# Kernel optimization log

Measured on AMD Instinct MI355X. Metric: run time of the kernel, lower is better.

The kernel has to match this reference:

```python
import jax, jax.numpy as jnp
import numpy as np


def _sobel(img):
    # replicate-pad then Sobel cross-correlation (matches torch conv2d with wx, wy)
    p = jnp.pad(img, ((0, 0), (0, 0), (1, 1), (1, 1)), mode='edge')
    dx = ((p[:, :, 0:-2, 2:] - p[:, :, 0:-2, 0:-2])
          + 2.0 * (p[:, :, 1:-1, 2:] - p[:, :, 1:-1, 0:-2])
          + (p[:, :, 2:, 2:] - p[:, :, 2:, 0:-2]))
    dy = ((p[:, :, 2:, 0:-2] - p[:, :, 0:-2, 0:-2])
          + 2.0 * (p[:, :, 2:, 1:-1] - p[:, :, 0:-2, 1:-1])
          + (p[:, :, 2:, 2:] - p[:, :, 0:-2, 2:]))
    return dx, dy


def _compute_normal(vertex):
    # normal = normalize(dV/dx x dV/dy); zero out pixels at global min/max depth
    dx, dy = _sobel(vertex)
    n = jnp.cross(dx, dy, axis=1)                      # [B,3,H,W]
    mag = jnp.sqrt(jnp.sum(n * n, axis=1, keepdims=True) + 1e-16)
    n = n / (mag + 1e-8)
    depth = vertex[:, 2:3]
    invalid = (depth == depth.min()) | (depth == depth.max())
    return jnp.where(invalid, 0.0, n)


def _warp(feat, u, v):
    # bilinear sampling of feat [B,C,H,W] at (u,v) [B,N] -> [B,C,N]
    B, C, H, W = feat.shape
    u = jnp.clip(u, 0.0, W - 1.0)
    v = jnp.clip(v, 0.0, H - 1.0)
    u0 = jnp.floor(u); v0 = jnp.floor(v)
    wu = u - u0; wv = v - v0
    u0i = u0.astype(jnp.int32); v0i = v0.astype(jnp.int32)
    u1i = jnp.minimum(u0i + 1, W - 1); v1i = jnp.minimum(v0i + 1, H - 1)
    flat = feat.reshape(B, C, H * W)
    N = u.shape[-1]
    def g(ui, vi):
        idx = (vi * W + ui)[:, None, :]
        return jnp.take_along_axis(flat, jnp.broadcast_to(idx, (B, C, N)), axis=2)
    return (g(u0i, v0i) * ((1 - wu) * (1 - wv))[:, None]
            + g(u1i, v0i) * (wu * (1 - wv))[:, None]
            + g(u0i, v1i) * ((1 - wu) * wv)[:, None]
            + g(u1i, v1i) * (wu * wv)[:, None])


def _skew(v):  # [B,3] -> [B,3,3]
    x, y, z = v[..., 0], v[..., 1], v[..., 2]
    O = jnp.zeros_like(x)
    return jnp.stack([jnp.stack([O, -z, y], -1),
                      jnp.stack([z, O, -x], -1),
                      jnp.stack([-y, x, O], -1)], -2)


def _twist2mat(w):  # Rodrigues: so(3) [B,3] -> SO(3) [B,3,3]
    th = jnp.sqrt(jnp.sum(w * w, -1, keepdims=True) + 1e-24)
    Kv = _skew(w / th)
    th = th[..., None]
    I = jnp.eye(3, dtype=w.dtype)
    return I + jnp.sin(th) * Kv + (1.0 - jnp.cos(th)) * (Kv @ Kv)


def _icp_forward(depth0, depth1, K, R, t, max_iter=3):
    B, _, H, W = depth0.shape
    fx, fy, cx, cy = [K[:, i:i + 1] for i in range(4)]  # each [B,1]
    uu = jnp.arange(W, dtype=depth0.dtype)
    vv = jnp.arange(H, dtype=depth0.dtype)
    px = (uu[None, None, None, :] - cx[:, :, None, None]) / fx[:, :, None, None]
    py = (vv[None, None, :, None] - cy[:, :, None, None]) / fy[:, :, None, None]
    px = jnp.broadcast_to(px, (B, 1, H, W))
    py = jnp.broadcast_to(py, (B, 1, H, W))
    vertex0 = jnp.concatenate([px * depth0, py * depth0, depth0], 1)  # [B,3,H,W]
    vertex1 = jnp.concatenate([px * depth1, py * depth1, depth1], 1)
    normal0 = _compute_normal(vertex0)
    normal1 = _compute_normal(vertex1)
    N = H * W
    V0 = vertex0.reshape(B, 3, N)
    N0 = normal0.reshape(B, 3, N)
    P0 = V0.transpose(0, 2, 1)                          # [B,N,3]
    dpt0 = vertex0[:, 2].reshape(B, N)
    sigma_z = 0.0012 + 0.0019 * (dpt0 - 0.4) ** 2       # depth noise model
    eye6 = jnp.eye(6, dtype=depth0.dtype)
    for _ in range(max_iter):
        v0to1 = R @ V0 + t                               # [B,3,N]
        x_, y_, s_ = v0to1[:, 0], v0to1[:, 1], v0to1[:, 2]
        u_ = x_ / s_ * fx + cx
        v_ = y_ / s_ * fy + cy
        inviews = (u_ > 0) & (u_ < W - 1) & (v_ > 0) & (v_ < H - 1)
        rV1 = _warp(vertex1, u_, v_)                     # [B,3,N]
        rN1 = _warp(normal1, u_, v_)
        diff = v0to1 - rV1
        dnorm = jnp.sqrt(jnp.sum(diff * diff, axis=1) + 1e-16)
        occ = (~inviews) | (dnorm > 0.1)                 # [B,N]
        res = jnp.sum(rN1 * diff, axis=1)                # point-to-plane residual [B,N]
        NtC = jnp.einsum('bcn,bck->bnk', rN1, R)         # n_r^T R, [B,N,3]
        # n^T [p]_x == cross(n^T R, p)
        J = jnp.concatenate([jnp.cross(NtC, P0), -NtC], -1)  # [B,N,6]
        # sigma ~ |n_r . (R e_z)| * sigma_z (depth noise projected on normal)
        ndot = jnp.abs(jnp.sum(rN1 * R[:, :, 2][:, :, None], axis=1))
        sigma = ndot * sigma_z + 1e-3
        w_res = res / (sigma + 1e-8)
        J = -J / (sigma + 1e-8)[..., None]
        w_res = jnp.where(occ, 0.0, w_res)
        J = jnp.where(occ[..., None], 0.0, J)
        JtWJ = jnp.einsum('bnk,bnl->bkl', J, J)          # [B,6,6]
        JtR = jnp.einsum('bnk,bn->bk', J, w_res)[..., None]  # [B,6,1]
        tr = jnp.trace(JtWJ, axis1=1, axis2=2)
        Hlm = JtWJ + (tr * 1e-6)[:, None, None] * eye6   # LM damping
        xi = jnp.linalg.inv(Hlm) @ JtR                   # [B,6,1]
        dR = _twist2mat(-xi[:, :3, 0])
        dt = -(dR @ xi[:, 3:])
        R, t = R @ dR, R @ dt + t                        # inverse-compositional update
    weights = jnp.ones((B, 1, H, W), dtype=depth0.dtype)
    return R, t, weights


def setup_inputs() -> dict:
    key = jax.random.key(0)
    B, H, W = 16, 480, 640
    k1, k2, k3, k4 = jax.random.split(key, 4)
    TWO_PI = 6.2831853
    xs = jnp.linspace(0.0, 1.0, W, dtype=jnp.float32)
    ys = jnp.linspace(0.0, 1.0, H, dtype=jnp.float32)
    phase = jax.random.uniform(k1, (B, 1, 1, 1), minval=0.0, maxval=TWO_PI)
    # smooth positive depth surface so ICP inlier test keeps valid pixels
    depth0 = (2.0 + 0.5 * jnp.sin(TWO_PI * 3.0 * xs[None, None, None, :] + phase)
              * jnp.cos(TWO_PI * 2.0 * ys[None, None, :, None])).astype(jnp.float32)
    depth1 = depth0 + 0.01 * jax.random.normal(k2, (B, 1, H, W), dtype=jnp.float32)
    K = jnp.tile(jnp.array([[525.0, 525.0, 319.5, 239.5]], dtype=jnp.float32), (B, 1))
    w = 0.005 * jax.random.normal(k3, (B, 3), dtype=jnp.float32)
    R = _twist2mat(w)                                    # near-identity initial rotation
    t = 0.005 * jax.random.normal(k4, (B, 3, 1), dtype=jnp.float32)
    return {"depth0": depth0, "depth1": depth1, "K": K, "R": R, "t": t}


def reference(depth0, depth1, K, R, t):
    return _icp_forward(depth0, depth1, K, R, t, max_iter=3)
```

## Files before the change

### kernel.cpp

```cpp
#include <hip/hip_runtime.h>

#define IMH 480
#define IMW 640
#define HW (IMH*IMW)
#define NB 16

#define BPB 100
#define TPX 4
#define GROUPS 3
#define THREADS_PB (BPB*256)
#define GSTRIDE (THREADS_PB*TPX)
#define GROWS (GSTRIDE/IMW)

#define MMB 512

__device__ inline unsigned fenc(float x){
    unsigned u = __float_as_uint(x);
    return (u & 0x80000000u) ? ~u : (u | 0x80000000u);
}
__device__ inline float fdec(unsigned e){
    unsigned u = (e & 0x80000000u) ? (e & 0x7FFFFFFFu) : ~e;
    return __uint_as_float(u);
}

__global__ __launch_bounds__(256) void minmax_kernel(const float4* __restrict__ d,
                                                     unsigned* __restrict__ pmin,
                                                     unsigned* __restrict__ pmax,
                                                     float* __restrict__ acc){
    if (blockIdx.x == 0){
        for (int k = threadIdx.x; k < NB*27; k += 256) acc[k] = 0.f;
    }
    unsigned lmin = 0xFFFFFFFFu, lmax = 0u;
    const int total4 = NB*HW/4;
    for (int i = blockIdx.x*256 + threadIdx.x; i < total4; i += MMB*256){
        float4 v = d[i];
        unsigned e0 = fenc(v.x), e1 = fenc(v.y), e2 = fenc(v.z), e3 = fenc(v.w);
        lmin = min(lmin, min(min(e0,e1), min(e2,e3)));
        lmax = max(lmax, max(max(e0,e1), max(e2,e3)));
    }
    #pragma unroll
    for (int off = 32; off; off >>= 1){
        lmin = min(lmin, (unsigned)__shfl_down((int)lmin, off));
        lmax = max(lmax, (unsigned)__shfl_down((int)lmax, off));
    }
    __shared__ unsigned smin[4], smax[4];
    int wave = threadIdx.x >> 6, lane = threadIdx.x & 63;
    if (lane == 0){ smin[wave] = lmin; smax[wave] = lmax; }
    __syncthreads();
    if (threadIdx.x == 0){
        pmin[blockIdx.x] = min(min(smin[0],smin[1]), min(smin[2],smin[3]));
        pmax[blockIdx.x] = max(max(smax[0],smax[1]), max(smax[2],smax[3]));
    }
}

__global__ __launch_bounds__(256) void normal_kernel(const float* __restrict__ depth1,
                                                     const float* __restrict__ Kp,
                                                     const unsigned* __restrict__ pmin,
                                                     const unsigned* __restrict__ pmax,
                                                     uint4* __restrict__ nrm4,
                                                     float4* __restrict__ weights4){
    __shared__ unsigned sred[8];
    __shared__ unsigned sfin[2];
    {
        unsigned vmin = min(pmin[threadIdx.x], pmin[threadIdx.x + 256]);
        unsigned vmax = max(pmax[threadIdx.x], pmax[threadIdx.x + 256]);
        #pragma unroll
        for (int off = 32; off; off >>= 1){
            vmin = min(vmin, (unsigned)__shfl_down((int)vmin, off));
            vmax = max(vmax, (unsigned)__shfl_down((int)vmax, off));
        }
        int wave = threadIdx.x >> 6, lane = threadIdx.x & 63;
        if (lane == 0){ sred[wave] = vmin; sred[4+wave] = vmax; }
        __syncthreads();
        if (threadIdx.x == 0){
            sfin[0] = min(min(sred[0],sred[1]), min(sred[2],sred[3]));
            sfin[1] = max(max(sred[4],sred[5]), max(sred[6],sred[7]));
        }
        __syncthreads();
    }
    const float dmin = fdec(sfin[0]), dmax = fdec(sfin[1]);

    const int b = blockIdx.y;
    const int t = blockIdx.x*256 + threadIdx.x;
    const int gpr = IMW/4;
    const int r = t / gpr;
    const int c0 = (t - r*gpr)*4;
    const float fx = Kp[b*4+0], fy = Kp[b*4+1], cx = Kp[b*4+2], cy = Kp[b*4+3];
    const float inv_fx = 1.f/fx, inv_fy = 1.f/fy;
    const float* __restrict__ d = depth1 + (size_t)b*HW;
    const int rm = max(r-1,0), rp = min(r+1,IMH-1);

    float wm[6], wc[6], wp[6];
    {
        const float* rowm = d + rm*IMW + c0;
        const float* rowc = d + r *IMW + c0;
        const float* rowp = d + rp*IMW + c0;
        float4 vm = *(const float4*)rowm;
        float4 vc = *(const float4*)rowc;
        float4 vp = *(const float4*)rowp;
        wm[1]=vm.x; wm[2]=vm.y; wm[3]=vm.z; wm[4]=vm.w;
        wc[1]=vc.x; wc[2]=vc.y; wc[3]=vc.z; wc[4]=vc.w;
        wp[1]=vp.x; wp[2]=vp.y; wp[3]=vp.z; wp[4]=vp.w;
        bool hasL = (c0 > 0), hasR = (c0+4 < IMW);
        wm[0] = hasL ? rowm[-1] : vm.x;   wm[5] = hasR ? rowm[4] : vm.w;
        wc[0] = hasL ? rowc[-1] : vc.x;   wc[5] = hasR ? rowc[4] : vc.w;
        wp[0] = hasL ? rowp[-1] : vp.x;   wp[5] = hasR ? rowp[4] : vp.w;
    }
    float pxw[6];
    #pragma unroll
    for (int k=0;k<6;k++){
        int cc = min(max(c0-1+k, 0), IMW-1);
        pxw[k] = ((float)cc - cx)*inv_fx;
    }
    const float pym = ((float)rm - cy)*inv_fy;
    const float pyc = ((float)r  - cy)*inv_fy;
    const float pyp = ((float)rp - cy)*inv_fy;

    unsigned packed[4];
    #pragma unroll
    for (int j=0;j<4;j++){
        float aL = wm[j],  aC = wm[j+1], aR = wm[j+2];
        float bL = wc[j],               bR = wc[j+2];
        float cL = wp[j],  cC = wp[j+1], cR = wp[j+2];
        float pL = pxw[j], pC = pxw[j+1], pR = pxw[j+2];

        float dx0 = (pR*aR - pL*aL) + 2.f*(pR*bR - pL*bL) + (pR*cR - pL*cL);
        float dx1 = pym*(aR - aL) + 2.f*pyc*(bR - bL) + pyp*(cR - cL);
        float dx2 = (aR - aL) + 2.f*(bR - bL) + (cR - cL);
        float dy0 = pL*(cL - aL) + 2.f*pC*(cC - aC) + pR*(cR - aR);
        float dy1 = (pyp*cL - pym*aL) + 2.f*(pyp*cC - pym*aC) + (pyp*cR - pym*aR);
        float dy2 = (cL - aL) + 2.f*(cC - aC) + (cR - aR);

        float nx = dx1*dy2 - dx2*dy1;
        float ny = dx2*dy0 - dx0*dy2;
        float nz = dx0*dy1 - dx1*dy0;
        float mag = sqrtf(nx*nx + ny*ny + nz*nz + 1e-16f);
        float inv = __builtin_amdgcn_rcpf(mag + 1e-8f);
        nx *= inv; ny *= inv; nz *= inv;

        float dc = wc[j+1];
        if (dc == dmin || dc == dmax){ nx = 0.f; ny = 0.f; nz = 0.f; }

        int qx = (int)rintf(nx*127.f) + 127;
        int qy = (int)rintf(ny*127.f) + 127;
        int qz = (int)rintf(nz*127.f) + 127;
        packed[j] = ((unsigned)qx) | ((unsigned)qy << 8) | ((unsigned)qz << 16);
    }

    size_t o4 = (size_t)b*(HW/4) + (size_t)r*gpr + (c0>>2);
    nrm4[o4] = make_uint4(packed[0], packed[1], packed[2], packed[3]);
    weights4[o4] = make_float4(1.f,1.f,1.f,1.f);
}

__global__ __launch_bounds__(256) void iter_kernel(const float4* __restrict__ depth0_v4,
                                                   const float* __restrict__ depth1,
                                                   const unsigned* __restrict__ nrm,
                                                   const float* __restrict__ Kp,
                                                   const float* __restrict__ stateR,
                                                   const float* __restrict__ statet,
                                                   float* __restrict__ acc){
    const int b = blockIdx.y;
    const float fx = Kp[b*4+0], fy = Kp[b*4+1], cx = Kp[b*4+2], cy = Kp[b*4+3];
    const float inv_fx = 1.f/fx, inv_fy = 1.f/fy;
    float Rm[9];
    #pragma unroll
    for (int i=0;i<9;i++) Rm[i] = stateR[b*9+i];
    float tv[3];
    #pragma unroll
    for (int i=0;i<3;i++) tv[i] = statet[b*3+i];

    const float4* __restrict__ d0v = depth0_v4 + (size_t)b*(HW/4);
    const float* __restrict__ d1   = depth1 + (size_t)b*HW;
    const unsigned* __restrict__ nb_ = nrm + (size_t)b*HW;

    float accv[27];
    #pragma unroll
    for (int i=0;i<27;i++) accv[i] = 0.f;

    const int tid = blockIdx.x*256 + threadIdx.x;
    const int base0 = tid*TPX;
    const int c0 = base0 % IMW;
    const int r0 = base0 / IMW;
    const float px_base = ((float)c0 - cx)*inv_fx;
    const float py0 = ((float)r0 - cy)*inv_fy;
    const float py_step = (float)GROWS*inv_fy;
    const float inv127 = 1.f/127.f;

    #pragma unroll
    for (int g = 0; g < GROUPS; g++){
        float4 d4 = d0v[tid + g*THREADS_PB];
        float dd[4] = {d4.x, d4.y, d4.z, d4.w};
        float pyv = py0 + (float)g*py_step;

        #pragma unroll
        for (int j = 0; j < TPX; j++){
            float d0 = dd[j];
            float V0x = (px_base + (float)j*inv_fx)*d0;
            float V0y = pyv*d0;
            float V0z = d0;

            float X = Rm[0]*V0x + Rm[1]*V0y + Rm[2]*V0z + tv[0];
            float Y = Rm[3]*V0x + Rm[4]*V0y + Rm[5]*V0z + tv[1];
            float Z = Rm[6]*V0x + Rm[7]*V0y + Rm[8]*V0z + tv[2];
            float invZ = __builtin_amdgcn_rcpf(Z);
            float uu = X*invZ*fx + cx;
            float vv = Y*invZ*fy + cy;

            bool inview = (uu > 0.f) && (uu < (float)(IMW-1)) && (vv > 0.f) && (vv < (float)(IMH-1));

            float J0=0.f,J1=0.f,J2=0.f,J3=0.f,J4=0.f,J5=0.f,wres=0.f;
            if (inview){
                float u0f = floorf(uu), v0f = floorf(vv);
                int u0 = (int)u0f, v0 = (int)v0f;
                float wu = uu - u0f, wv = vv - v0f;
                float w00 = (1.f-wu)*(1.f-wv), w10 = wu*(1.f-wv), w01 = (1.f-wu)*wv, w11 = wu*wv;
                int i00 = v0*IMW + u0;

                float d00 = d1[i00], d10 = d1[i00+1], d01 = d1[i00+IMW], d11 = d1[i00+IMW+1];
                unsigned h00 = nb_[i00], h10 = nb_[i00+1], h01 = nb_[i00+IMW], h11 = nb_[i00+IMW+1];

                float pxa = (u0f - cx)*inv_fx, pxb = pxa + inv_fx;
                float pya = (v0f - cy)*inv_fy, pyb = pya + inv_fy;
                float a = w00*d00, bb = w10*d10, cc = w01*d01, ee = w11*d11;
                float rVz = (a + bb) + (cc + ee);
                float rVx = (a + cc)*pxa + (bb + ee)*pxb;
                float rVy = (a + bb)*pya + (cc + ee)*pyb;

                float q00x = (float)(h00 & 0xFFu);
                float q00y = (float)((h00 >> 8) & 0xFFu);
                float q00z = (float)((h00 >> 16) & 0xFFu);
                float q10x = (float)(h10 & 0xFFu);
                float q10y = (float)((h10 >> 8) & 0xFFu);
                float q10z = (float)((h10 >> 16) & 0xFFu);
                float q01x = (float)(h01 & 0xFFu);
                float q01y = (float)((h01 >> 8) & 0xFFu);
                float q01z = (float)((h01 >> 16) & 0xFFu);
                float q11x = (float)(h11 & 0xFFu);
                float q11y = (float)((h11 >> 8) & 0xFFu);
                float q11z = (float)((h11 >> 16) & 0xFFu);

                float n0x = ((w00*q00x + w10*q10x + w01*q01x + w11*q11x) - 127.f) * inv127;
                float n0y = ((w00*q00y + w10*q10y + w01*q01y + w11*q11y) - 127.f) * inv127;
                float n0z = ((w00*q00z + w10*q10z + w01*q01z + w11*q11z) - 127.f) * inv127;

                float dfx = X - rVx, dfy = Y - rVy, dfz = Z - rVz;
                float d2 = dfx*dfx + dfy*dfy + dfz*dfz + 1e-16f;
                if (d2 <= 0.01f){
                    float res = n0x*dfx + n0y*dfy + n0z*dfz;
                    float N0 = n0x*Rm[0] + n0y*Rm[3] + n0z*Rm[6];
                    float N1 = n0x*Rm[1] + n0y*Rm[4] + n0z*Rm[7];
                    float N2 = n0x*Rm[2] + n0y*Rm[5] + n0z*Rm[8];
                    float cr0 = N1*V0z - N2*V0y;
                    float cr1 = N2*V0x - N0*V0z;
                    float cr2 = N0*V0y - N1*V0x;
                    float ndot = fabsf(N2);
                    float dsh = d0 - 0.4f;
                    float sigz = 0.0012f + 0.0019f*dsh*dsh;
                    float sigma = ndot*sigz + 0.001f;
                    float invs = __builtin_amdgcn_rcpf(sigma + 1e-8f);
                    wres = res*invs;
                    J0 = -cr0*invs; J1 = -cr1*invs; J2 = -cr2*invs;
                    J3 =  N0*invs;  J4 =  N1*invs;  J5 =  N2*invs;
                }
            }

            float Jv[6] = {J0,J1,J2,J3,J4,J5};
            int idx = 0;
            #pragma unroll
            for (int k=0;k<6;k++)
                #pragma unroll
                for (int l=k;l<6;l++){ accv[idx] += Jv[k]*Jv[l]; idx++; }
            #pragma unroll
            for (int k=0;k<6;k++){ accv[idx] += Jv[k]*wres; idx++; }
        }
    }

    #pragma unroll
    for (int i=0;i<27;i++){
        float v = accv[i];
        #pragma unroll
        for (int off=32; off; off >>= 1) v += __shfl_down(v, off);
        accv[i] = v;
    }

    __shared__ float sacc[4][27];
    int wave = threadIdx.x >> 6, lane = threadIdx.x & 63;
    if (lane == 0){
        #pragma unroll
        for (int i=0;i<27;i++) sacc[wave][i] = accv[i];
    }
    __syncthreads();
    if (threadIdx.x < 27){
        float s = sacc[0][threadIdx.x] + sacc[1][threadIdx.x]
                + sacc[2][threadIdx.x] + sacc[3][threadIdx.x];
        atomicAdd(&acc[b*27 + threadIdx.x], s);
    }
}

__global__ void solve_kernel(float* __restrict__ acc,
                             const float* __restrict__ prevR, const float* __restrict__ prevT,
                             float* __restrict__ stateR, float* __restrict__ statet,
                             float* __restrict__ outR, float* __restrict__ outt){
    int b = threadIdx.x;
    if (b >= NB) return;

    float a27[27];
    #pragma unroll
    for (int i=0;i<27;i++) a27[i] = acc[b*27+i];
    #pragma unroll
    for (int i=0;i<27;i++) acc[b*27+i] = 0.f;

    float A[6][6], rhs[6];
    int idx = 0;
    #pragma unroll
    for (int k=0;k<6;k++)
        #pragma unroll
        for (int l=k;l<6;l++){ A[k][l] = a27[idx]; A[l][k] = a27[idx]; idx++; }
    #pragma unroll
    for (int k=0;k<6;k++) rhs[k] = a27[21+k];

    float tr = 0.f;
    #pragma unroll
    for (int k=0;k<6;k++) tr += A[k][k];
    float lm = tr*1e-6f;
    #pragma unroll
    for (int k=0;k<6;k++) A[k][k] += lm;

    float L[6][6];
    #pragma unroll
    for (int i=0;i<6;i++){
        #pragma unroll
        for (int j=0;j<=i;j++){
            float s = A[i][j];
            #pragma unroll
            for (int k=0;k<j;k++) s -= L[i][k]*L[j][k];
            if (i == j) L[i][i] = sqrtf(s);
            else        L[i][j] = s / L[j][j];
        }
    }
    float y[6];
    #pragma unroll
    for (int i=0;i<6;i++){
        float s = rhs[i];
        #pragma unroll
        for (int k=0;k<i;k++) s -= L[i][k]*y[k];
        y[i] = s / L[i][i];
    }
    float xi[6];
    #pragma unroll
    for (int ii=5; ii>=0; ii--){
        float s = y[ii];
        #pragma unroll
        for (int k=ii+1;k<6;k++) s -= L[k][ii]*xi[k];
        xi[ii] = s / L[ii][ii];
    }

    float w0 = -xi[0], w1 = -xi[1], w2 = -xi[2];
    float th = sqrtf(w0*w0 + w1*w1 + w2*w2 + 1e-24f);
    float ith = 1.f/th;
    float kx = w0*ith, ky = w1*ith, kz = w2*ith;
    float s = sinf(th), cm1 = 1.f - cosf(th);
    float dRm[9];
    dRm[0] = 1.f + cm1*(-ky*ky - kz*kz);
    dRm[1] = -s*kz + cm1*(kx*ky);
    dRm[2] =  s*ky + cm1*(kx*kz);
    dRm[3] =  s*kz + cm1*(kx*ky);
    dRm[4] = 1.f + cm1*(-kx*kx - kz*kz);
    dRm[5] = -s*kx + cm1*(ky*kz);
    dRm[6] = -s*ky + cm1*(kx*kz);
    dRm[7] =  s*kx + cm1*(ky*kz);
    dRm[8] = 1.f + cm1*(-kx*kx - ky*ky);

    float dt0 = -(dRm[0]*xi[3] + dRm[1]*xi[4] + dRm[2]*xi[5]);
    float dt1 = -(dRm[3]*xi[3] + dRm[4]*xi[4] + dRm[5]*xi[5]);
    float dt2 = -(dRm[6]*xi[3] + dRm[7]*xi[4] + dRm[8]*xi[5]);

    float Rm[9], tv[3];
    #pragma unroll
    for (int i=0;i<9;i++) Rm[i] = prevR[b*9+i];
    #pragma unroll
    for (int i=0;i<3;i++) tv[i] = prevT[b*3+i];

    float Rn[9];
    #pragma unroll
    for (int i=0;i<3;i++)
        #pragma unroll
        for (int j=0;j<3;j++)
            Rn[i*3+j] = Rm[i*3+0]*dRm[0*3+j] + Rm[i*3+1]*dRm[1*3+j] + Rm[i*3+2]*dRm[2*3+j];
    float tn0 = Rm[0]*dt0 + Rm[1]*dt1 + Rm[2]*dt2 + tv[0];
    float tn1 = Rm[3]*dt0 + Rm[4]*dt1 + Rm[5]*dt2 + tv[1];
    float tn2 = Rm[6]*dt0 + Rm[7]*dt1 + Rm[8]*dt2 + tv[2];

    #pragma unroll
    for (int i=0;i<9;i++){ stateR[b*9+i] = Rn[i]; outR[b*9+i] = Rn[i]; }
    statet[b*3+0] = tn0; outt[b*3+0] = tn0;
    statet[b*3+1] = tn1; outt[b*3+1] = tn1;
    statet[b*3+2] = tn2; outt[b*3+2] = tn2;
}

extern "C" void kernel_launch(void* const* d_in, const int* in_sizes, int n_in,
                              void* d_out, int out_size, void* d_ws, size_t ws_size,
                              hipStream_t stream){
    const float* depth0 = (const float*)d_in[0];
    const float* depth1 = (const float*)d_in[1];
    const float* Kp     = (const float*)d_in[2];
    const float* Rin    = (const float*)d_in[3];
    const float* tin    = (const float*)d_in[4];

    float* out     = (float*)d_out;
    float* outR    = out;
    float* outt    = out + NB*9;
    float* weights = out + NB*12;

    unsigned* nrm  = (unsigned*)d_ws;
    unsigned* pmin = nrm + (size_t)NB*HW;
    unsigned* pmax = pmin + MMB;
    float* stateR  = (float*)(pmax + MMB);
    float* statet  = stateR + NB*9;
    float* acc     = statet + NB*3;

    minmax_kernel<<<dim3(MMB), 256, 0, stream>>>((const float4*)depth1, pmin, pmax, acc);
    normal_kernel<<<dim3(HW/4/256, NB), 256, 0, stream>>>(depth1, Kp, pmin, pmax, (uint4*)nrm, (float4*)weights);
    for (int it = 0; it < 3; it++){
        const float* Rsrc = (it == 0) ? Rin : stateR;
        const float* tsrc = (it == 0) ? tin : statet;
        iter_kernel<<<dim3(BPB, NB), 256, 0, stream>>>((const float4*)depth0, depth1, nrm, Kp, Rsrc, tsrc, acc);
        solve_kernel<<<1, 64, 0, stream>>>(acc, Rsrc, tsrc, stateR, statet, outR, outt);
    }
}
```

Measured before the change: 226.9 us.

## Store depth1 and normals in 2x2 quad-tiled layout for vectorized bilinear gathers

Minmax now also writes depth1 into a 2x2 quad-interleaved copy, and normal_kernel writes normals in the same quad layout. The iteration kernel fetches bilinear neighbors as float4/uint4 quads, loading one to four quads depending on alignment parity instead of eight scalar gathers. This aims to cut memory transactions in the gather-heavy ICP loop. In exchange it adds an extra full-size write pass over depth1, more workspace, and branchy parity selection logic.

```diff
diff --git a/kernel.cpp b/kernel.cpp
--- a/kernel.cpp
+++ b/kernel.cpp
@@ -4,6 +4,7 @@
 #define IMW 640
 #define HW (IMH*IMW)
 #define NB 16
+#define QPR (IMW/2)
 
 #define BPB 100
 #define TPX 4
@@ -23,7 +24,8 @@
     return __uint_as_float(u);
 }
 
-__global__ __launch_bounds__(256) void minmax_kernel(const float4* __restrict__ d,
+__global__ __launch_bounds__(256) void minmax_kernel(const float* __restrict__ d,
+                                                     float* __restrict__ d1q,
                                                      unsigned* __restrict__ pmin,
                                                      unsigned* __restrict__ pmax,
                                                      float* __restrict__ acc){
@@ -31,12 +33,20 @@
         for (int k = threadIdx.x; k < NB*27; k += 256) acc[k] = 0.f;
     }
     unsigned lmin = 0xFFFFFFFFu, lmax = 0u;
-    const int total4 = NB*HW/4;
-    for (int i = blockIdx.x*256 + threadIdx.x; i < total4; i += MMB*256){
-        float4 v = d[i];
-        unsigned e0 = fenc(v.x), e1 = fenc(v.y), e2 = fenc(v.z), e3 = fenc(v.w);
-        lmin = min(lmin, min(min(e0,e1), min(e2,e3)));
-        lmax = max(lmax, max(max(e0,e1), max(e2,e3)));
+    const int total = NB*HW/8;
+    for (int i = blockIdx.x*256 + threadIdx.x; i < total; i += MMB*256){
+        int rp   = i / (IMW/4);
+        int col4 = i - rp*(IMW/4);
+        const float* top = d + (size_t)rp*(2*IMW) + col4*4;
+        float4 t = *(const float4*)top;
+        float4 bt = *(const float4*)(top + IMW);
+        unsigned e0=fenc(t.x),e1=fenc(t.y),e2=fenc(t.z),e3=fenc(t.w);
+        unsigned f0=fenc(bt.x),f1=fenc(bt.y),f2=fenc(bt.z),f3=fenc(bt.w);
+        lmin = min(lmin, min(min(min(e0,e1),min(e2,e3)), min(min(f0,f1),min(f2,f3))));
+        lmax = max(lmax, max(max(max(e0,e1),max(e2,e3)), max(max(f0,f1),max(f2,f3))));
+        float* dst = d1q + (size_t)rp*(2*IMW) + col4*8;
+        *(float4*)dst       = make_float4(t.x, t.y, bt.x, bt.y);
+        *(float4*)(dst + 4) = make_float4(t.z, t.w, bt.z, bt.w);
     }
     #pragma unroll
     for (int off = 32; off; off >>= 1){
@@ -57,7 +67,7 @@
                                                      const float* __restrict__ Kp,
                                                      const unsigned* __restrict__ pmin,
                                                      const unsigned* __restrict__ pmax,
-                                                     uint4* __restrict__ nrm4,
+                                                     unsigned* __restrict__ nrmq,
                                                      float4* __restrict__ weights4){
     __shared__ unsigned sred[8];
     __shared__ unsigned sfin[2];
@@ -147,14 +157,17 @@
         packed[j] = ((unsigned)qx) | ((unsigned)qy << 8) | ((unsigned)qz << 16);
     }
 
+    size_t qb = (size_t)b*HW + (size_t)(r>>1)*(2*IMW) + (size_t)(c0>>1)*4 + (size_t)(r&1)*2;
+    *(uint2*)(nrmq + qb)     = make_uint2(packed[0], packed[1]);
+    *(uint2*)(nrmq + qb + 4) = make_uint2(packed[2], packed[3]);
+
     size_t o4 = (size_t)b*(HW/4) + (size_t)r*gpr + (c0>>2);
-    nrm4[o4] = make_uint4(packed[0], packed[1], packed[2], packed[3]);
     weights4[o4] = make_float4(1.f,1.f,1.f,1.f);
 }
 
 __global__ __launch_bounds__(256) void iter_kernel(const float4* __restrict__ depth0_v4,
-                                                   const float* __restrict__ depth1,
-                                                   const unsigned* __restrict__ nrm,
+                                                   const float4* __restrict__ d1q,
+                                                   const uint4* __restrict__ nrmq,
                                                    const float* __restrict__ Kp,
                                                    const float* __restrict__ stateR,
                                                    const float* __restrict__ statet,
@@ -170,8 +183,8 @@
     for (int i=0;i<3;i++) tv[i] = statet[b*3+i];
 
     const float4* __restrict__ d0v = depth0_v4 + (size_t)b*(HW/4);
-    const float* __restrict__ d1   = depth1 + (size_t)b*HW;
-    const unsigned* __restrict__ nb_ = nrm + (size_t)b*HW;
+    const float4* __restrict__ dq  = d1q + (size_t)b*(HW/4);
+    const uint4*  __restrict__ nq  = nrmq + (size_t)b*(HW/4);
 
     float accv[27];
     #pragma unroll
@@ -214,10 +227,34 @@
                 int u0 = (int)u0f, v0 = (int)v0f;
                 float wu = uu - u0f, wv = vv - v0f;
                 float w00 = (1.f-wu)*(1.f-wv), w10 = wu*(1.f-wv), w01 = (1.f-wu)*wv, w11 = wu*wv;
-                int i00 = v0*IMW + u0;
-
-                float d00 = d1[i00], d10 = d1[i00+1], d01 = d1[i00+IMW], d11 = d1[i00+IMW+1];
-                unsigned h00 = nb_[i00], h10 = nb_[i00+1], h01 = nb_[i00+IMW], h11 = nb_[i00+IMW+1];
+
+                int u0h = u0 >> 1, aq = u0 & 1;
+                int v0h = v0 >> 1, bq = v0 & 1;
+                int qi = v0h*QPR + u0h;
+
+                float4 D00 = dq[qi];
+                float4 DR = D00, DD = D00;
+                if (aq) DR = dq[qi+1];
+                if (bq) DD = dq[qi+QPR];
+                float4 DRD = aq ? DR : DD;
+                if (aq & bq) DRD = dq[qi+QPR+1];
+
+                float d00 = bq ? (aq ? D00.w : D00.z) : (aq ? D00.y : D00.x);
+                float d10 = aq ? (bq ? DR.z : DR.x)   : (bq ? D00.w : D00.y);
+                float d01 = bq ? (aq ? DD.y : DD.x)   : (aq ? D00.w : D00.z);
+                float d11 = bq ? (aq ? DRD.x : DD.y)  : (aq ? DR.z : D00.w);
+
+                uint4 N00 = nq[qi];
+                uint4 NR = N00, ND = N00;
+                if (aq) NR = nq[qi+1];
+                if (bq) ND = nq[qi+QPR];
+                uint4 NRD = aq ? NR : ND;
+                if (aq & bq) NRD = nq[qi+QPR+1];
+
+                unsigned h00 = bq ? (aq ? N00.w : N00.z) : (aq ? N00.y : N00.x);
+                unsigned h10 = aq ? (bq ? NR.z : NR.x)   : (bq ? N00.w : N00.y);
+                unsigned h01 = bq ? (aq ? ND.y : ND.x)   : (aq ? N00.w : N00.z);
+                unsigned h11 = bq ? (aq ? NRD.x : ND.y)  : (aq ? NR.z : N00.w);
 
                 float pxa = (u0f - cx)*inv_fx, pxb = pxa + inv_fx;
                 float pya = (v0f - cy)*inv_fy, pyb = pya + inv_fy;
@@ -412,19 +449,21 @@
     float* outt    = out + NB*9;
     float* weights = out + NB*12;
 
-    unsigned* nrm  = (unsigned*)d_ws;
-    unsigned* pmin = nrm + (size_t)NB*HW;
+    unsigned* nrmq = (unsigned*)d_ws;
+    float* d1q     = (float*)(nrmq + (size_t)NB*HW);
+    unsigned* pmin = (unsigned*)(d1q + (size_t)NB*HW);
     unsigned* pmax = pmin + MMB;
     float* stateR  = (float*)(pmax + MMB);
     float* statet  = stateR + NB*9;
     float* acc     = statet + NB*3;
 
-    minmax_kernel<<<dim3(MMB), 256, 0, stream>>>((const float4*)depth1, pmin, pmax, acc);
-    normal_kernel<<<dim3(HW/4/256, NB), 256, 0, stream>>>(depth1, Kp, pmin, pmax, (uint4*)nrm, (float4*)weights);
+    minmax_kernel<<<dim3(MMB), 256, 0, stream>>>(depth1, d1q, pmin, pmax, acc);
+    normal_kernel<<<dim3(HW/4/256, NB), 256, 0, stream>>>(depth1, Kp, pmin, pmax, nrmq, (float4*)weights);
     for (int it = 0; it < 3; it++){
         const float* Rsrc = (it == 0) ? Rin : stateR;
         const float* tsrc = (it == 0) ? tin : statet;
-        iter_kernel<<<dim3(BPB, NB), 256, 0, stream>>>((const float4*)depth0, depth1, nrm, Kp, Rsrc, tsrc, acc);
+        iter_kernel<<<dim3(BPB, NB), 256, 0, stream>>>((const float4*)depth0, (const float4*)d1q, (const uint4*)nrmq,
+                                                       Kp, Rsrc, tsrc, acc);
         solve_kernel<<<1, 64, 0, stream>>>(acc, Rsrc, tsrc, stateR, statet, outR, outt);
     }
 }
```

Result: slower. 302.2 us (+33.2%).
